# Optimization experiments

Measured on AMD Instinct MI355X. Metric: run time of the kernel, lower is better.

Reference implementation:

```python
import jax, jax.numpy as jnp
import numpy as np

B, D, H, W = 16, 512, 32, 32   # batch, input_dim, spatial
CD, K = 256, 8192              # codebook dim, num codes
COMMIT = 1.0


def setup_inputs() -> dict:
    key = jax.random.key(0)
    k0, k1, k2, k3 = jax.random.split(key, 4)
    x = jax.random.normal(k0, (B, D, H, W), dtype=jnp.float32)
    # project_in: Linear(D -> CD); project_out: Linear(CD -> D)
    W_in = jax.random.normal(k1, (CD, D), dtype=jnp.float32) * (1.0 / np.sqrt(D))
    b_in = jnp.zeros((CD,), dtype=jnp.float32)
    W_out = jax.random.normal(k2, (D, CD), dtype=jnp.float32) * (1.0 / np.sqrt(CD))
    b_out = jnp.zeros((D,), dtype=jnp.float32)
    codebook = jax.random.normal(k3, (K, CD), dtype=jnp.float32) * 0.05
    return {"x": x, "W_in": W_in, "b_in": b_in, "W_out": W_out,
            "b_out": b_out, "codebook": codebook}


def reference(x, W_in, b_in, W_out, b_out, codebook):
    b, d, h, w = x.shape
    # b d h w -> b (h w) d
    xt = x.reshape(b, d, h * w).transpose(0, 2, 1)
    z = xt @ W_in.T + b_in                              # [b, n, CD]
    # squared euclidean distances to all codes: ||z||^2 - 2 z.e + ||e||^2
    d2 = ((z * z).sum(-1, keepdims=True)
          - 2.0 * jnp.einsum('bnc,kc->bnk', z, codebook)
          + (codebook * codebook).sum(-1))              # [b, n, K]
    indices = jnp.argmin(d2, axis=-1)                   # [b, n] int
    q = codebook[indices]                               # [b, n, CD]
    # training branch: commitment loss + straight-through estimator
    commitment_loss = COMMIT * jnp.mean((jax.lax.stop_gradient(q) - z) ** 2)
    q_ste = z + jax.lax.stop_gradient(q - z)
    out = q_ste @ W_out.T + b_out                       # [b, n, d]
    out = out.transpose(0, 2, 1).reshape(b, d, h, w)    # b (h w) d -> b d h w
    return out, indices, commitment_loss
```

## Files before the change

kernel.cpp:

```cpp
#include <hip/hip_runtime.h>
#include <cfloat>
#include <cstdint>

#define B_      16
#define DIN     512
#define HW      1024
#define CDIM    256
#define KCODES  8192
#define NTOK    (B_ * HW)
#define OUT_ELEMS (B_ * DIN * HW)
#define NSTRIP  8
#define NPART2  16
#define CPS     (KCODES / NSTRIP)
#define MAXR    4096
#define RCHUNK  32
#define RBLOCKS 2048
#define LOSS_SCALE (1.0f / ((float)NTOK * (float)CDIM))
#define WSCALE      16.0f
#define INV_WS      0.0625f
#define INV_WS2     0.00390625f
#define NEG2_INV_WS (-0.125f)
#define BAND_SLACK  2e-3f
#define A_BYTES  131072
#define B_OFF    131072
#define EE_OFF   (131072 + 3 * 8192)
#define LDS_TOT  (EE_OFF + 4096)
#define PO_BOFF  65536
#define PO_TOT   163840

typedef __attribute__((ext_vector_type(8))) _Float16 f16x8;
typedef __attribute__((ext_vector_type(4))) float f32x4;

static __device__ __forceinline__ short f2h(float f) {
  _Float16 h = (_Float16)f;
  return __builtin_bit_cast(short, h);
}
static __device__ __forceinline__ float h2f(short h) {
  return (float)__builtin_bit_cast(_Float16, h);
}

#define GLL16(gsrc, ldst)                                                      \
  __builtin_amdgcn_global_load_lds(                                           \
      (const __attribute__((address_space(1))) unsigned int*)(gsrc),          \
      (__attribute__((address_space(3))) unsigned int*)(ldst), 16, 0, 0)

#define PREP_CB_BLKS 2048
#define PREP_W_BLKS  128
#define PREP_X_BLKS  2048
__global__ __launch_bounds__(256) void k_prep(
    const float* __restrict__ cb, const float* __restrict__ Win,
    const float* __restrict__ Wout, const float* __restrict__ x,
    short* __restrict__ cb_hi, short* __restrict__ cb_lo, float* __restrict__ ee,
    short* __restrict__ wi_hi, short* __restrict__ wi_lo,
    short* __restrict__ wo_hi,
    short* __restrict__ xT_hi, short* __restrict__ xT_lo,
    float* __restrict__ loss, int* __restrict__ rcount, int* __restrict__ scal) {
  __shared__ float T[64][65];
  const int blk = blockIdx.x;
  const int tid = threadIdx.x;
  if (blk == 0 && tid < 2) {
    if (tid == 0) *loss = 0.0f; else *rcount = 0;
  }
  if (blk < PREP_CB_BLKS) {
    const int wid = (blk * 256 + tid) >> 6;
    const int lane = tid & 63;
    const float4 v = *(const float4*)(cb + (size_t)wid * CDIM + lane * 4);
    float s = v.x * v.x + v.y * v.y + v.z * v.z + v.w * v.w;
    const float sx = v.x * WSCALE, sy = v.y * WSCALE,
                sz = v.z * WSCALE, sw = v.w * WSCALE;
    short4 h, l;
    h.x = f2h(sx); l.x = f2h(sx - h2f(h.x));
    h.y = f2h(sy); l.y = f2h(sy - h2f(h.y));
    h.z = f2h(sz); l.z = f2h(sz - h2f(h.z));
    h.w = f2h(sw); l.w = f2h(sw - h2f(h.w));
    *(short4*)(cb_hi + (size_t)wid * CDIM + lane * 4) = h;
    *(short4*)(cb_lo + (size_t)wid * CDIM + lane * 4) = l;
    const float rx = v.x - h2f(h.x) * INV_WS;
    const float ry = v.y - h2f(h.y) * INV_WS;
    const float rz = v.z - h2f(h.z) * INV_WS;
    const float rw = v.w - h2f(h.w) * INV_WS;
    float rr = rx * rx + ry * ry + rz * rz + rw * rw;
#pragma unroll
    for (int off = 32; off > 0; off >>= 1) {
      s += __shfl_down(s, off, 64);
      rr += __shfl_down(rr, off, 64);
    }
    const int wv = tid >> 6;
    if (lane == 0) { ee[wid] = s; T[0][wv] = s; T[1][wv] = rr; }
    __syncthreads();
    if (tid == 0) {
      const float em = fmaxf(fmaxf(T[0][0], T[0][1]), fmaxf(T[0][2], T[0][3]));
      const float rm = fmaxf(fmaxf(T[1][0], T[1][1]), fmaxf(T[1][2], T[1][3]));
      atomicMax(scal + 0, __float_as_int(em));
      atomicMax(scal + 1, __float_as_int(rm));
    }
  } else if (blk < PREP_CB_BLKS + PREP_W_BLKS) {
    const int i = ((blk - PREP_CB_BLKS) * 256 + tid) * 4;
    {
      const float4 v = *(const float4*)(Win + i);
      const float sx = v.x * WSCALE, sy = v.y * WSCALE,
                  sz = v.z * WSCALE, sw = v.w * WSCALE;
      short4 h, l;
      h.x = f2h(sx); l.x = f2h(sx - h2f(h.x));
      h.y = f2h(sy); l.y = f2h(sy - h2f(h.y));
      h.z = f2h(sz); l.z = f2h(sz - h2f(h.z));
      h.w = f2h(sw); l.w = f2h(sw - h2f(h.w));
      *(short4*)(wi_hi + i) = h; *(short4*)(wi_lo + i) = l;
    }
    {
      const float4 v = *(const float4*)(Wout + i);
      short4 h;
      h.x = f2h(v.x * WSCALE);
      h.y = f2h(v.y * WSCALE);
      h.z = f2h(v.z * WSCALE);
      h.w = f2h(v.w * WSCALE);
      *(short4*)(wo_hi + i) = h;
    }
  } else {
    const int id = blk - PREP_CB_BLKS - PREP_W_BLKS;
    const int xb = id & 255, yb = id >> 8;
    const int b = xb >> 4;
    const int hw0 = (xb & 15) * 64;
    const int din0 = yb * 64;
    {
      const int r = tid >> 2;
      const int c = tid & 3;
      const float* src = x + ((size_t)b * DIN + din0 + r) * HW + hw0 + c * 16;
#pragma unroll
      for (int j = 0; j < 4; ++j) {
        const float4 v = *(const float4*)(src + j * 4);
        T[r][c * 16 + j * 4 + 0] = v.x;
        T[r][c * 16 + j * 4 + 1] = v.y;
        T[r][c * 16 + j * 4 + 2] = v.z;
        T[r][c * 16 + j * 4 + 3] = v.w;
      }
    }
    __syncthreads();
    {
      const int tt = tid & 63;
      const int c2 = tid >> 6;
      short h[16], l[16];
#pragma unroll
      for (int j = 0; j < 16; ++j) {
        const float f = T[c2 * 16 + j][tt];
        h[j] = f2h(f); l[j] = f2h(f - h2f(h[j]));
      }
      const size_t base = ((size_t)b * HW + hw0 + tt) * DIN + din0 + c2 * 16;
      *(f16x8*)(xT_hi + base)     = *(f16x8*)&h[0];
      *(f16x8*)(xT_hi + base + 8) = *(f16x8*)&h[8];
      *(f16x8*)(xT_lo + base)     = *(f16x8*)&l[0];
      *(f16x8*)(xT_lo + base + 8) = *(f16x8*)&l[8];
    }
  }
}

__global__ __launch_bounds__(256, 2) void k_proj_in_mfma(
    const short* __restrict__ xT_hi, const short* __restrict__ xT_lo,
    const short* __restrict__ wi_hi, const short* __restrict__ wi_lo,
    const float* __restrict__ bin,
    short* __restrict__ z_hi, short* __restrict__ z_lo) {
  __shared__ short lds_s[3 * 16384];
  char* ldsc = (char*)lds_s;
  const int tid = threadIdx.x;
  const int w = tid >> 6, lane = tid & 63;
  const int quad = lane >> 4, l16 = lane & 15;
  const int wm = w >> 1, wn = w & 1;
  const int tok0 = blockIdx.x * 128;
  const int cd0 = blockIdx.y * 128;

  const int t0 = tid >> 2, p0 = tid & 3, q0 = p0 ^ ((t0 >> 1) & 3);
  const int u1 = tid + 256, t1 = u1 >> 2, p1 = u1 & 3, q1 = p1 ^ ((t1 >> 1) & 3);
  const short* A0h = xT_hi + (size_t)(tok0 + t0) * DIN + q0 * 8;
  const short* A1h = xT_hi + (size_t)(tok0 + t1) * DIN + q1 * 8;
  const short* A0l = xT_lo + (size_t)(tok0 + t0) * DIN + q0 * 8;
  const short* A1l = xT_lo + (size_t)(tok0 + t1) * DIN + q1 * 8;
  const short* B0h = wi_hi + (size_t)(cd0 + t0) * DIN + q0 * 8;
  const short* B1h = wi_hi + (size_t)(cd0 + t1) * DIN + q1 * 8;
  const short* B0l = wi_lo + (size_t)(cd0 + t0) * DIN + q0 * 8;
  const short* B1l = wi_lo + (size_t)(cd0 + t1) * DIN + q1 * 8;

#define PI_STAGE(s_, slot_)                                                    \
  {                                                                            \
    char* bb_ = ldsc + ((slot_) << 15);                                        \
    const int kb_ = (s_) * 32;                                                 \
    GLL16(A0h + kb_, bb_ + (w << 10));                                         \
    GLL16(A1h + kb_, bb_ + 4096 + (w << 10));                                  \
    GLL16(A0l + kb_, bb_ + 8192 + (w << 10));                                  \
    GLL16(A1l + kb_, bb_ + 12288 + (w << 10));                                 \
    GLL16(B0h + kb_, bb_ + 16384 + (w << 10));                                 \
    GLL16(B1h + kb_, bb_ + 20480 + (w << 10));                                 \
    GLL16(B0l + kb_, bb_ + 24576 + (w << 10));                                 \
    GLL16(B1l + kb_, bb_ + 28672 + (w << 10));                                 \
  }
  PI_STAGE(0, 0);
  PI_STAGE(1, 1);

  int aoffs[4], boffs[4];
#pragma unroll
  for (int mi = 0; mi < 4; ++mi) {
    const int t = wm * 64 + mi * 16 + l16;
    aoffs[mi] = t * 64 + (quad ^ ((t >> 1) & 3)) * 16;
  }
#pragma unroll
  for (int ni = 0; ni < 4; ++ni) {
    const int t = wn * 64 + ni * 16 + l16;
    boffs[ni] = 16384 + t * 64 + (quad ^ ((t >> 1) & 3)) * 16;
  }

  f32x4 acc[4][4];
#pragma unroll
  for (int mi = 0; mi < 4; ++mi)
#pragma unroll
    for (int ni = 0; ni < 4; ++ni) acc[mi][ni] = (f32x4){0.f, 0.f, 0.f, 0.f};

  int cur = 0;
#pragma unroll
  for (int s = 0; s < 16; ++s) {
    asm volatile("s_waitcnt vmcnt(8)" ::: "memory");
    __builtin_amdgcn_s_barrier();
    __builtin_amdgcn_sched_barrier(0);
    {
      const int s2 = (s + 2) & 15;
      const int nslot = cur + 2 - ((cur >= 1) ? 3 : 0);
      PI_STAGE(s2, nslot);
    }
    const int bb = cur << 15;
    f16x8 ah[4], al[4], bh[4], bl[4];
#pragma unroll
    for (int mi = 0; mi < 4; ++mi) {
      ah[mi] = *(const f16x8*)(ldsc + bb + aoffs[mi]);
      al[mi] = *(const f16x8*)(ldsc + bb + 8192 + aoffs[mi]);
    }
#pragma unroll
    for (int ni = 0; ni < 4; ++ni) {
      bh[ni] = *(const f16x8*)(ldsc + bb + boffs[ni]);
      bl[ni] = *(const f16x8*)(ldsc + bb + 8192 + boffs[ni]);
    }
    __builtin_amdgcn_s_setprio(1);
#pragma unroll
    for (int mi = 0; mi < 4; ++mi)
#pragma unroll
      for (int ni = 0; ni < 4; ++ni) {
        f32x4 c = acc[mi][ni];
        c = __builtin_amdgcn_mfma_f32_16x16x32_f16(ah[mi], bh[ni], c, 0, 0, 0);
        c = __builtin_amdgcn_mfma_f32_16x16x32_f16(ah[mi], bl[ni], c, 0, 0, 0);
        c = __builtin_amdgcn_mfma_f32_16x16x32_f16(al[mi], bh[ni], c, 0, 0, 0);
        acc[mi][ni] = c;
      }
    __builtin_amdgcn_s_setprio(0);
    cur = (cur == 2) ? 0 : cur + 1;
  }
#undef PI_STAGE

  float bv[4];
#pragma unroll
  for (int ni = 0; ni < 4; ++ni) bv[ni] = bin[cd0 + wn * 64 + ni * 16 + l16];
#pragma unroll
  for (int mi = 0; mi < 4; ++mi)
#pragma unroll
    for (int r = 0; r < 4; ++r) {
      const int t = tok0 + wm * 64 + mi * 16 + quad * 4 + r;
#pragma unroll
      for (int ni = 0; ni < 4; ++ni) {
        const int cd = cd0 + wn * 64 + ni * 16 + l16;
        const float o = acc[mi][ni][r] * INV_WS + bv[ni];
        const short h = f2h(o);
        z_hi[(size_t)t * CDIM + cd] = h;
        z_lo[(size_t)t * CDIM + cd] = f2h(o - h2f(h));
      }
    }
}

__global__ __launch_bounds__(512, 2) void k_argmin_mfma(
    const short* __restrict__ z_hi,
    const short* __restrict__ cb_hi,
    const float* __restrict__ ee,
    float* __restrict__ pm1v, int* __restrict__ pm1i, float* __restrict__ pm2v) {
  __shared__ short lds_s[LDS_TOT / 2];
  char* ldsc = (char*)lds_s;
  const int tid = threadIdx.x;
  const int w = tid >> 6, lane = tid & 63;
  const int quad = lane >> 4, l16 = lane & 15;
  const int wm = w >> 1, wn = w & 1;
  const int tok0 = blockIdx.x * 256;
  const int cbase = blockIdx.y * CPS;

#pragma unroll
  for (int r = 0; r < 16; ++r) {
    const int u = r * 512 + tid;
    const int c = u >> 10, t = (u >> 2) & 255, p = u & 3;
    const int q = p ^ ((t >> 1) & 3);
    GLL16(z_hi + (size_t)(tok0 + t) * CDIM + c * 32 + q * 8,
          ldsc + r * 8192 + (w << 10));
  }
  if (w < 4) {
    GLL16(ee + cbase + w * 256 + lane * 4, ldsc + EE_OFF + (w << 10));
  }
  const int crB = tid >> 2, pB = tid & 3;
  const int qB = pB ^ ((crB >> 1) & 3);
  const short* bsrc = cb_hi + (size_t)(cbase + crB) * CDIM + qB * 8;
  GLL16(bsrc, ldsc + B_OFF + (w << 10));
  GLL16(bsrc + 32, ldsc + B_OFF + 8192 + (w << 10));

  int aoffs[4], boffs[4];
#pragma unroll
  for (int mi = 0; mi < 4; ++mi) {
    const int t = wm * 64 + mi * 16 + l16;
    aoffs[mi] = t * 64 + (quad ^ ((t >> 1) & 3)) * 16;
  }
#pragma unroll
  for (int ni = 0; ni < 4; ++ni) {
    const int t = wn * 64 + ni * 16 + l16;
    boffs[ni] = t * 64 + (quad ^ ((t >> 1) & 3)) * 16;
  }
  const float* eelds = (const float*)(ldsc + EE_OFF);

  float mv[16], sv[16]; int mi_[16];
#pragma unroll
  for (int j = 0; j < 16; ++j) {
    mv[j] = FLT_MAX; sv[j] = FLT_MAX; mi_[j] = 0x7fffffff;
  }

  int cur = 0;
  for (int ct = 0; ct < 8; ++ct) {
    f32x4 acc[4][4];
#pragma unroll
    for (int mi = 0; mi < 4; ++mi)
#pragma unroll
      for (int ni = 0; ni < 4; ++ni) acc[mi][ni] = (f32x4){0.f, 0.f, 0.f, 0.f};

#pragma unroll
    for (int kbi = 0; kbi < 8; ++kbi) {
      const int s = ct * 8 + kbi;
      asm volatile("s_waitcnt vmcnt(1)" ::: "memory");
      __builtin_amdgcn_s_barrier();
      __builtin_amdgcn_sched_barrier(0);
      {
        const int s2 = (s + 2) & 63;
        const int nslot = cur + 2 - ((cur >= 1) ? 3 : 0);
        GLL16(bsrc + (size_t)(s2 >> 3) * 128 * CDIM + (s2 & 7) * 32,
              ldsc + B_OFF + (nslot << 13) + (w << 10));
      }
      const int abase = kbi << 14;
      const int bbase = B_OFF + (cur << 13);
      f16x8 ah[4], bh[4];
#pragma unroll
      for (int mi = 0; mi < 4; ++mi)
        ah[mi] = *(const f16x8*)(ldsc + abase + aoffs[mi]);
#pragma unroll
      for (int ni = 0; ni < 4; ++ni)
        bh[ni] = *(const f16x8*)(ldsc + bbase + boffs[ni]);
      __builtin_amdgcn_s_setprio(1);
#pragma unroll
      for (int mi = 0; mi < 4; ++mi)
#pragma unroll
        for (int ni = 0; ni < 4; ++ni)
          acc[mi][ni] = __builtin_amdgcn_mfma_f32_16x16x32_f16(
              ah[mi], bh[ni], acc[mi][ni], 0, 0, 0);
      __builtin_amdgcn_s_setprio(0);
      cur = (cur == 2) ? 0 : cur + 1;
    }
    const int ctile = cbase + ct * 128;
    float eev[4];
#pragma unroll
    for (int ni = 0; ni < 4; ++ni)
      eev[ni] = eelds[ct * 128 + wn * 64 + ni * 16 + l16];
    const int cb2 = ctile + wn * 64 + l16;
#pragma unroll
    for (int mi = 0; mi < 4; ++mi)
#pragma unroll
      for (int r = 0; r < 4; ++r) {
        const int j = mi * 4 + r;
#pragma unroll
        for (int ni = 0; ni < 4; ++ni) {
          const float s = fmaf(NEG2_INV_WS, acc[mi][ni][r], eev[ni]);
          sv[j] = fminf(sv[j], fmaxf(mv[j], s));
          if (s < mv[j]) { mv[j] = s; mi_[j] = cb2 + ni * 16; }
        }
      }
  }
#pragma unroll
  for (int off = 1; off < 16; off <<= 1) {
#pragma unroll
    for (int j = 0; j < 16; ++j) {
      const float ov = __shfl_xor(mv[j], off, 64);
      const int   oi = __shfl_xor(mi_[j], off, 64);
      const float os = __shfl_xor(sv[j], off, 64);
      const float snew = fminf(fminf(sv[j], os), fmaxf(mv[j], ov));
      if (ov < mv[j] || (ov == mv[j] && oi < mi_[j])) { mv[j] = ov; mi_[j] = oi; }
      sv[j] = snew;
    }
  }
  if (l16 == 0) {
    const int p = blockIdx.y * 2 + wn;
#pragma unroll
    for (int j = 0; j < 16; ++j) {
      const int mi = j >> 2, r = j & 3;
      const int t = tok0 + wm * 64 + mi * 16 + quad * 4 + r;
      const size_t o = (size_t)p * NTOK + t;
      pm1v[o] = mv[j]; pm1i[o] = mi_[j]; pm2v[o] = sv[j];
    }
  }
}

__global__ __launch_bounds__(256) void k_merge_rescue(
    const float* __restrict__ pm1v, const int* __restrict__ pm1i,
    const float* __restrict__ pm2v,
    const short* __restrict__ z_hi, const short* __restrict__ z_lo,
    const float* __restrict__ cb, const int* __restrict__ scal,
    int* __restrict__ idxi, float* __restrict__ idx_f,
    int* __restrict__ rlist, int* __restrict__ rcount,
    float* __restrict__ loss) {
  __shared__ float lpart[4];
  const int tid = threadIdx.x;
  const int wv = tid >> 6, lane = tid & 63;
  const int t = blockIdx.x * 4 + wv;
  float av = FLT_MAX, asv = FLT_MAX; int ai = 0x7fffffff;
  if (lane < NPART2) {
    const size_t po = (size_t)lane * NTOK + t;
    av = pm1v[po]; ai = pm1i[po]; asv = pm2v[po];
  }
  float m1v = av; int m1i = ai; float msv = asv;
#pragma unroll
  for (int off = 1; off < 64; off <<= 1) {
    const float ov = __shfl_xor(m1v, off, 64);
    const int   oi = __shfl_xor(m1i, off, 64);
    const float os = __shfl_xor(msv, off, 64);
    msv = fminf(msv, os);
    if (ov < m1v || (ov == m1v && oi < m1i)) { m1v = ov; m1i = oi; }
  }
  const short4 h4 = *(const short4*)(z_hi + (size_t)t * CDIM + lane * 4);
  const short4 l4 = *(const short4*)(z_lo + (size_t)t * CDIM + lane * 4);
  const float hx = h2f(h4.x), hy = h2f(h4.y), hz = h2f(h4.z), hw = h2f(h4.w);
  const float lx = h2f(l4.x), ly = h2f(l4.y), lz = h2f(l4.z), lw = h2f(l4.w);
  const float zx = hx + lx, zy = hy + ly, zz = hz + lz, zw = hw + lw;
  float zl2 = lx * lx + ly * ly + lz * lz + lw * lw;
  float zh2 = hx * hx + hy * hy + hz * hz + hw * hw;
#pragma unroll
  for (int off = 32; off > 0; off >>= 1) {
    zl2 += __shfl_xor(zl2, off, 64);
    zh2 += __shfl_xor(zh2, off, 64);
  }
  const float emax = sqrtf(__int_as_float(scal[0]));
  const float rmax = sqrtf(__int_as_float(scal[1]));
  const float band = 4.0f * (sqrtf(zl2) * emax + sqrtf(zh2) * rmax) + BAND_SLACK;
  const float thr = m1v + band;
  const unsigned long long ball = __ballot(av <= thr);
  const bool flag = (msv <= thr);
  int besti = m1i;
  if (__popcll(ball) > 1) {
    double bestv = 1e300; int bi = 0x7fffffff;
    unsigned long long bb = ball;
    while (bb) {
      const int c = __ffsll((long long)bb) - 1;
      bb &= bb - 1;
      const int ci = __shfl(ai, c, 64);
      const float4 ev = *(const float4*)(cb + (size_t)ci * CDIM + lane * 4);
      const double dx = (double)zx - (double)ev.x;
      const double dy = (double)zy - (double)ev.y;
      const double dz_ = (double)zz - (double)ev.z;
      const double dw = (double)zw - (double)ev.w;
      double d = dx * dx + dy * dy + dz_ * dz_ + dw * dw;
#pragma unroll
      for (int off = 32; off > 0; off >>= 1) d += __shfl_xor(d, off, 64);
      if (d < bestv || (d == bestv && ci < bi)) { bestv = d; bi = ci; }
    }
    besti = bi;
  }
  const float4 qv = *(const float4*)(cb + (size_t)besti * CDIM + lane * 4);
  const float dx = qv.x - zx;
  const float dy = qv.y - zy;
  const float dz_ = qv.z - zz;
  const float dw = qv.w - zw;
  float s = dx * dx + dy * dy + dz_ * dz_ + dw * dw;
#pragma unroll
  for (int off = 32; off > 0; off >>= 1) s += __shfl_down(s, off, 64);
  if (lane == 0) {
    idxi[t] = besti;
    idx_f[t] = (float)besti;
    lpart[wv] = s;
    if (flag) {
      const int pos = atomicAdd(rcount, 1);
      if (pos < MAXR) rlist[pos] = t;
    }
  }
  __syncthreads();
  if (tid == 0) {
    atomicAdd(loss, (lpart[0] + lpart[1] + lpart[2] + lpart[3]) * LOSS_SCALE);
  }
}

__global__ __launch_bounds__(256) void k_rescue_chunk(
    const short* __restrict__ z_hi, const short* __restrict__ z_lo,
    const float* __restrict__ cb,
    const int* __restrict__ rlist, const int* __restrict__ rcount,
    double* __restrict__ slotv, int* __restrict__ sloti) {
  const int cnt0 = *rcount;
  const int cnt = cnt0 < MAXR ? cnt0 : MAXR;
  const int li0 = blockIdx.x >> 5;
  const int chunk = blockIdx.x & (RCHUNK - 1);
  if (li0 >= cnt) return;
  __shared__ float zrow[CDIM];
  __shared__ double rv[256];
  __shared__ int ri[256];
  const int tid = threadIdx.x;
  for (int li = li0; li < cnt; li += RBLOCKS / RCHUNK) {
    const int t = rlist[li];
    zrow[tid] = h2f(z_hi[(size_t)t * CDIM + tid]) + h2f(z_lo[(size_t)t * CDIM + tid]);
    __syncthreads();
    const int k = chunk * 256 + tid;
    const float* e = cb + (size_t)k * CDIM;
    double s0 = 0.0, s1 = 0.0, s2 = 0.0, s3 = 0.0;
    for (int c = 0; c < CDIM; c += 4) {
      const float4 ev = *(const float4*)(e + c);
      const double d0 = (double)zrow[c]     - (double)ev.x;
      const double d1 = (double)zrow[c + 1] - (double)ev.y;
      const double d2 = (double)zrow[c + 2] - (double)ev.z;
      const double d3 = (double)zrow[c + 3] - (double)ev.w;
      s0 += d0 * d0; s1 += d1 * d1; s2 += d2 * d2; s3 += d3 * d3;
    }
    rv[tid] = (s0 + s1) + (s2 + s3);
    ri[tid] = k;
    __syncthreads();
    for (int off = 128; off > 0; off >>= 1) {
      if (tid < off) {
        if (rv[tid + off] < rv[tid] ||
            (rv[tid + off] == rv[tid] && ri[tid + off] < ri[tid])) {
          rv[tid] = rv[tid + off]; ri[tid] = ri[tid + off];
        }
      }
      __syncthreads();
    }
    if (tid == 0) {
      slotv[(size_t)li * RCHUNK + chunk] = rv[0];
      sloti[(size_t)li * RCHUNK + chunk] = ri[0];
    }
    __syncthreads();
  }
}

__global__ __launch_bounds__(256) void k_rescue_fin(
    const double* __restrict__ slotv, const int* __restrict__ sloti,
    const int* __restrict__ rlist, const int* __restrict__ rcount,
    const short* __restrict__ z_hi, const short* __restrict__ z_lo,
    const float* __restrict__ cb,
    int* __restrict__ idxi, float* __restrict__ idx_f, float* __restrict__ loss) {
  const int cnt0 = *rcount;
  const int cnt = cnt0 < MAXR ? cnt0 : MAXR;
  const int tid = threadIdx.x;
  const int wv = tid >> 6, lane = tid & 63;
  for (int li = wv; li < cnt; li += 4) {
    double bv = 1e300; int bx = 0x7fffffff;
    if (lane < RCHUNK) {
      bv = slotv[(size_t)li * RCHUNK + lane];
      bx = sloti[(size_t)li * RCHUNK + lane];
    }
#pragma unroll
    for (int off = 1; off < 32; off <<= 1) {
      const double ov = __shfl_xor(bv, off, 64);
      const int   oi = __shfl_xor(bx, off, 64);
      if (ov < bv || (ov == bv && oi < bx)) { bv = ov; bx = oi; }
    }
    const int newi = __shfl(bx, 0, 64);
    const int t = rlist[li];
    const int oldi = idxi[t];
    if (newi != oldi) {
      const short4 h4 = *(const short4*)(z_hi + (size_t)t * CDIM + lane * 4);
      const short4 l4 = *(const short4*)(z_lo + (size_t)t * CDIM + lane * 4);
      const float4 qn = *(const float4*)(cb + (size_t)newi * CDIM + lane * 4);
      const float4 qo = *(const float4*)(cb + (size_t)oldi * CDIM + lane * 4);
      const float zx = h2f(h4.x) + h2f(l4.x);
      const float zy = h2f(h4.y) + h2f(l4.y);
      const float zz = h2f(h4.z) + h2f(l4.z);
      const float zw = h2f(h4.w) + h2f(l4.w);
      float d = (qn.x - zx) * (qn.x - zx) - (qo.x - zx) * (qo.x - zx)
              + (qn.y - zy) * (qn.y - zy) - (qo.y - zy) * (qo.y - zy)
              + (qn.z - zz) * (qn.z - zz) - (qo.z - zz) * (qo.z - zz)
              + (qn.w - zw) * (qn.w - zw) - (qo.w - zw) * (qo.w - zw);
#pragma unroll
      for (int off = 32; off > 0; off >>= 1) d += __shfl_down(d, off, 64);
      if (lane == 0) {
        idxi[t] = newi;
        idx_f[t] = (float)newi;
        atomicAdd(loss, d * LOSS_SCALE);
      }
    }
  }
}

__global__ __launch_bounds__(512, 2) void k_proj_out_mfma(
    const short* __restrict__ wo_hi,
    const short* __restrict__ cb_hi, const short* __restrict__ cb_lo,
    const int* __restrict__ idxi, const float* __restrict__ bout,
    float* __restrict__ out) {
  __shared__ short lds_s[PO_TOT / 2];
  char* ldsc = (char*)lds_s;
  const int tid = threadIdx.x;
  const int w = tid >> 6, lane = tid & 63;
  const int quad = lane >> 4, l16 = lane & 15;
  const int wm = w >> 2, wn = w & 3;
  const int tok0 = blockIdx.x * 256;
  const int din0 = blockIdx.y * 128;

  const int tr = tid >> 2, p = tid & 3;
  const int q = p ^ ((tr >> 1) & 3);
  const int i0 = idxi[tok0 + tr];
  const int i1 = idxi[tok0 + 128 + tr];
  const short* s0h = cb_hi + (size_t)i0 * CDIM + q * 8;
  const short* s1h = cb_hi + (size_t)i1 * CDIM + q * 8;
  const short* s0l = cb_lo + (size_t)i0 * CDIM + q * 8;
  const short* s1l = cb_lo + (size_t)i1 * CDIM + q * 8;

#pragma unroll
  for (int c = 0; c < 8; ++c)
    GLL16(wo_hi + (size_t)(din0 + tr) * CDIM + c * 32 + q * 8,
          ldsc + c * 8192 + (w << 10));

#define PO_STAGE(s_, slot_)                                                    \
  {                                                                            \
    char* bb_ = ldsc + PO_BOFF + ((slot_) << 15);                              \
    GLL16(s0h + (s_) * 32, bb_ + (w << 10));                                   \
    GLL16(s1h + (s_) * 32, bb_ + 8192 + (w << 10));                            \
    GLL16(s0l + (s_) * 32, bb_ + 16384 + (w << 10));                           \
    GLL16(s1l + (s_) * 32, bb_ + 24576 + (w << 10));                           \
  }
  PO_STAGE(0, 0);
  PO_STAGE(1, 1);

  int aoffs[4], boffs[4];
#pragma unroll
  for (int mi = 0; mi < 4; ++mi) {
    const int t = wm * 64 + mi * 16 + l16;
    aoffs[mi] = t * 64 + (quad ^ ((t >> 1) & 3)) * 16;
  }
#pragma unroll
  for (int ni = 0; ni < 4; ++ni) {
    const int t = wn * 64 + ni * 16 + l16;
    boffs[ni] = t * 64 + (quad ^ ((t >> 1) & 3)) * 16;
  }

  f32x4 acc[4][4];
#pragma unroll
  for (int mi = 0; mi < 4; ++mi)
#pragma unroll
    for (int ni = 0; ni < 4; ++ni) acc[mi][ni] = (f32x4){0.f, 0.f, 0.f, 0.f};

  int cur = 0;
#pragma unroll
  for (int s = 0; s < 8; ++s) {
    asm volatile("s_waitcnt vmcnt(4)" ::: "memory");
    __builtin_amdgcn_s_barrier();
    __builtin_amdgcn_sched_barrier(0);
    {
      const int s2 = (s + 2) & 7;
      const int nslot = cur + 2 - ((cur >= 1) ? 3 : 0);
      PO_STAGE(s2, nslot);
    }
    const int abase = s << 13;
    const int bbase = PO_BOFF + (cur << 15);
    f16x8 ah[4], bh[4], bl[4];
#pragma unroll
    for (int mi = 0; mi < 4; ++mi)
      ah[mi] = *(const f16x8*)(ldsc + abase + aoffs[mi]);
#pragma unroll
    for (int ni = 0; ni < 4; ++ni) {
      bh[ni] = *(const f16x8*)(ldsc + bbase + boffs[ni]);
      bl[ni] = *(const f16x8*)(ldsc + bbase + 16384 + boffs[ni]);
    }
    __builtin_amdgcn_s_setprio(1);
#pragma unroll
    for (int mi = 0; mi < 4; ++mi)
#pragma unroll
      for (int ni = 0; ni < 4; ++ni) {
        f32x4 c = acc[mi][ni];
        c = __builtin_amdgcn_mfma_f32_16x16x32_f16(ah[mi], bh[ni], c, 0, 0, 0);
        c = __builtin_amdgcn_mfma_f32_16x16x32_f16(ah[mi], bl[ni], c, 0, 0, 0);
        acc[mi][ni] = c;
      }
    __builtin_amdgcn_s_setprio(0);
    cur = (cur == 2) ? 0 : cur + 1;
  }
#undef PO_STAGE

  const int b = tok0 >> 10;
  const int hwb = tok0 & (HW - 1);
  float* ob = out + (size_t)b * DIN * HW;
#pragma unroll
  for (int mi = 0; mi < 4; ++mi)
#pragma unroll
    for (int r = 0; r < 4; ++r) {
      const int din = din0 + wm * 64 + mi * 16 + quad * 4 + r;
      const float bb = bout[din];
#pragma unroll
      for (int ni = 0; ni < 4; ++ni) {
        const int hw = hwb + wn * 64 + ni * 16 + l16;
        ob[(size_t)din * HW + hw] = acc[mi][ni][r] * INV_WS2 + bb;
      }
    }
}

extern "C" void kernel_launch(void* const* d_in, const int* in_sizes, int n_in,
                              void* d_out, int out_size, void* d_ws, size_t ws_size,
                              hipStream_t stream) {
  const float* x    = (const float*)d_in[0];
  const float* Win  = (const float*)d_in[1];
  const float* bin  = (const float*)d_in[2];
  const float* Wout = (const float*)d_in[3];
  const float* bout = (const float*)d_in[4];
  const float* cb   = (const float*)d_in[5];

  float* out   = (float*)d_out;
  float* idx_f = out + OUT_ELEMS;
  float* loss  = out + OUT_ELEMS + NTOK;

  char* w = (char*)d_ws;
  size_t off = 0;
  short* z_hi  = (short*)(w + off); off += (size_t)NTOK * CDIM * 2;
  short* z_lo  = (short*)(w + off); off += (size_t)NTOK * CDIM * 2;
  short* cb_hi = (short*)(w + off); off += (size_t)KCODES * CDIM * 2;
  short* cb_lo = (short*)(w + off); off += (size_t)KCODES * CDIM * 2;
  short* xT_hi = (short*)(w + off); off += (size_t)NTOK * DIN * 2;
  short* xT_lo = (short*)(w + off); off += (size_t)NTOK * DIN * 2;
  short* wi_hi = (short*)(w + off); off += (size_t)CDIM * DIN * 2;
  short* wi_lo = (short*)(w + off); off += (size_t)CDIM * DIN * 2;
  short* wo_hi = (short*)(w + off); off += (size_t)DIN * CDIM * 2;
  float* ee    = (float*)(w + off); off += (size_t)KCODES * 4;
  int*   idxi  = (int*)(w + off);   off += (size_t)NTOK * 4;
  float* pm1v  = (float*)(w + off); off += (size_t)NPART2 * NTOK * 4;
  int*   pm1i  = (int*)(w + off);   off += (size_t)NPART2 * NTOK * 4;
  float* pm2v  = (float*)(w + off); off += (size_t)NPART2 * NTOK * 4;
  int*   rlist = (int*)(w + off);   off += (size_t)MAXR * 4;
  int*   rcount= (int*)(w + off);   off += 256;
  int*   scal  = (int*)(w + off);   off += 256;
  double* slotv= (double*)(w + off);off += (size_t)MAXR * RCHUNK * 8;
  int*   sloti = (int*)(w + off);   off += (size_t)MAXR * RCHUNK * 4;

  hipMemsetAsync(scal, 0, 8, stream);
  k_prep        <<<dim3(PREP_CB_BLKS + PREP_W_BLKS + PREP_X_BLKS),
                   dim3(256), 0, stream>>>(cb, Win, Wout, x, cb_hi, cb_lo, ee,
                                           wi_hi, wi_lo, wo_hi,
                                           xT_hi, xT_lo, loss, rcount, scal);
  k_proj_in_mfma<<<dim3(NTOK / 128, CDIM / 128), dim3(256), 0, stream>>>(
      xT_hi, xT_lo, wi_hi, wi_lo, bin, z_hi, z_lo);
  k_argmin_mfma <<<dim3(NTOK / 256, NSTRIP), dim3(512), 0, stream>>>(
      z_hi, cb_hi, ee, pm1v, pm1i, pm2v);
  k_merge_rescue<<<dim3(NTOK / 4), dim3(256), 0, stream>>>(
      pm1v, pm1i, pm2v, z_hi, z_lo, cb, scal, idxi, idx_f,
      rlist, rcount, loss);
  k_rescue_chunk<<<dim3(RBLOCKS), dim3(256), 0, stream>>>(
      z_hi, z_lo, cb, rlist, rcount, slotv, sloti);
  k_rescue_fin  <<<dim3(1), dim3(256), 0, stream>>>(
      slotv, sloti, rlist, rcount, z_hi, z_lo, cb, idxi, idx_f, loss);
  k_proj_out_mfma<<<dim3(NTOK / 256, DIN / 128), dim3(512), 0, stream>>>(
      wo_hi, cb_hi, cb_lo, idxi, bout, out);
}
```

Before: 429.9 us.

## Fuse rescue chunk and finalize kernels via last-block-done counter; drop setprio

```diff
diff --git a/kernel.cpp b/kernel.cpp
--- a/kernel.cpp
+++ b/kernel.cpp
@@ -54,12 +54,15 @@
     short* __restrict__ wi_hi, short* __restrict__ wi_lo,
     short* __restrict__ wo_hi,
     short* __restrict__ xT_hi, short* __restrict__ xT_lo,
-    float* __restrict__ loss, int* __restrict__ rcount, int* __restrict__ scal) {
+    float* __restrict__ loss, int* __restrict__ rcount,
+    int* __restrict__ done, int* __restrict__ scal) {
   __shared__ float T[64][65];
   const int blk = blockIdx.x;
   const int tid = threadIdx.x;
-  if (blk == 0 && tid < 2) {
-    if (tid == 0) *loss = 0.0f; else *rcount = 0;
+  if (blk == 0 && tid < 3) {
+    if (tid == 0) *loss = 0.0f;
+    else if (tid == 1) *rcount = 0;
+    else *done = 0;
   }
   if (blk < PREP_CB_BLKS) {
     const int wid = (blk * 256 + tid) >> 6;
@@ -350,14 +353,12 @@
 #pragma unroll
       for (int ni = 0; ni < 4; ++ni)
         bh[ni] = *(const f16x8*)(ldsc + bbase + boffs[ni]);
-      __builtin_amdgcn_s_setprio(1);
 #pragma unroll
       for (int mi = 0; mi < 4; ++mi)
 #pragma unroll
         for (int ni = 0; ni < 4; ++ni)
           acc[mi][ni] = __builtin_amdgcn_mfma_f32_16x16x32_f16(
               ah[mi], bh[ni], acc[mi][ni], 0, 0, 0);
-      __builtin_amdgcn_s_setprio(0);
       cur = (cur == 2) ? 0 : cur + 1;
     }
     const int ctile = cbase + ct * 128;
@@ -490,64 +491,63 @@
   }
 }
 
-__global__ __launch_bounds__(256) void k_rescue_chunk(
+__global__ __launch_bounds__(256) void k_rescue_fused(
     const short* __restrict__ z_hi, const short* __restrict__ z_lo,
     const float* __restrict__ cb,
     const int* __restrict__ rlist, const int* __restrict__ rcount,
-    double* __restrict__ slotv, int* __restrict__ sloti) {
+    double* __restrict__ slotv, int* __restrict__ sloti,
+    int* __restrict__ done,
+    int* __restrict__ idxi, float* __restrict__ idx_f,
+    float* __restrict__ loss) {
   const int cnt0 = *rcount;
   const int cnt = cnt0 < MAXR ? cnt0 : MAXR;
   const int li0 = blockIdx.x >> 5;
   const int chunk = blockIdx.x & (RCHUNK - 1);
-  if (li0 >= cnt) return;
   __shared__ float zrow[CDIM];
   __shared__ double rv[256];
   __shared__ int ri[256];
+  __shared__ int lastFlag;
   const int tid = threadIdx.x;
-  for (int li = li0; li < cnt; li += RBLOCKS / RCHUNK) {
-    const int t = rlist[li];
-    zrow[tid] = h2f(z_hi[(size_t)t * CDIM + tid]) + h2f(z_lo[(size_t)t * CDIM + tid]);
-    __syncthreads();
-    const int k = chunk * 256 + tid;
-    const float* e = cb + (size_t)k * CDIM;
-    double s0 = 0.0, s1 = 0.0, s2 = 0.0, s3 = 0.0;
-    for (int c = 0; c < CDIM; c += 4) {
-      const float4 ev = *(const float4*)(e + c);
-      const double d0 = (double)zrow[c]     - (double)ev.x;
-      const double d1 = (double)zrow[c + 1] - (double)ev.y;
-      const double d2 = (double)zrow[c + 2] - (double)ev.z;
-      const double d3 = (double)zrow[c + 3] - (double)ev.w;
-      s0 += d0 * d0; s1 += d1 * d1; s2 += d2 * d2; s3 += d3 * d3;
-    }
-    rv[tid] = (s0 + s1) + (s2 + s3);
-    ri[tid] = k;
-    __syncthreads();
-    for (int off = 128; off > 0; off >>= 1) {
-      if (tid < off) {
-        if (rv[tid + off] < rv[tid] ||
-            (rv[tid + off] == rv[tid] && ri[tid + off] < ri[tid])) {
-          rv[tid] = rv[tid + off]; ri[tid] = ri[tid + off];
+  if (li0 < cnt) {
+    for (int li = li0; li < cnt; li += RBLOCKS / RCHUNK) {
+      const int t = rlist[li];
+      zrow[tid] = h2f(z_hi[(size_t)t * CDIM + tid]) + h2f(z_lo[(size_t)t * CDIM + tid]);
+      __syncthreads();
+      const int k = chunk * 256 + tid;
+      const float* e = cb + (size_t)k * CDIM;
+      double s0 = 0.0, s1 = 0.0, s2 = 0.0, s3 = 0.0;
+      for (int c = 0; c < CDIM; c += 4) {
+        const float4 ev = *(const float4*)(e + c);
+        const double d0 = (double)zrow[c]     - (double)ev.x;
+        const double d1 = (double)zrow[c + 1] - (double)ev.y;
+        const double d2 = (double)zrow[c + 2] - (double)ev.z;
+        const double d3 = (double)zrow[c + 3] - (double)ev.w;
+        s0 += d0 * d0; s1 += d1 * d1; s2 += d2 * d2; s3 += d3 * d3;
+      }
+      rv[tid] = (s0 + s1) + (s2 + s3);
+      ri[tid] = k;
+      __syncthreads();
+      for (int off = 128; off > 0; off >>= 1) {
+        if (tid < off) {
+          if (rv[tid + off] < rv[tid] ||
+              (rv[tid + off] == rv[tid] && ri[tid + off] < ri[tid])) {
+            rv[tid] = rv[tid + off]; ri[tid] = ri[tid + off];
+          }
         }
+        __syncthreads();
+      }
+      if (tid == 0) {
+        slotv[(size_t)li * RCHUNK + chunk] = rv[0];
+        sloti[(size_t)li * RCHUNK + chunk] = ri[0];
       }
       __syncthreads();
     }
-    if (tid == 0) {
-      slotv[(size_t)li * RCHUNK + chunk] = rv[0];
-      sloti[(size_t)li * RCHUNK + chunk] = ri[0];
-    }
-    __syncthreads();
-  }
-}
-
-__global__ __launch_bounds__(256) void k_rescue_fin(
-    const double* __restrict__ slotv, const int* __restrict__ sloti,
-    const int* __restrict__ rlist, const int* __restrict__ rcount,
-    const short* __restrict__ z_hi, const short* __restrict__ z_lo,
-    const float* __restrict__ cb,
-    int* __restrict__ idxi, float* __restrict__ idx_f, float* __restrict__ loss) {
-  const int cnt0 = *rcount;
-  const int cnt = cnt0 < MAXR ? cnt0 : MAXR;
-  const int tid = threadIdx.x;
+  }
+  __threadfence();
+  if (tid == 0) lastFlag = (atomicAdd(done, 1) == RBLOCKS - 1);
+  __syncthreads();
+  if (lastFlag == 0) return;
+  __threadfence();
   const int wv = tid >> 6, lane = tid & 63;
   for (int li = wv; li < cnt; li += 4) {
     double bv = 1e300; int bx = 0x7fffffff;
@@ -731,6 +731,7 @@
   float* pm2v  = (float*)(w + off); off += (size_t)NPART2 * NTOK * 4;
   int*   rlist = (int*)(w + off);   off += (size_t)MAXR * 4;
   int*   rcount= (int*)(w + off);   off += 256;
+  int*   done  = (int*)(w + off);   off += 256;
   int*   scal  = (int*)(w + off);   off += 256;
   double* slotv= (double*)(w + off);off += (size_t)MAXR * RCHUNK * 8;
   int*   sloti = (int*)(w + off);   off += (size_t)MAXR * RCHUNK * 4;
@@ -739,7 +740,8 @@
   k_prep        <<<dim3(PREP_CB_BLKS + PREP_W_BLKS + PREP_X_BLKS),
                    dim3(256), 0, stream>>>(cb, Win, Wout, x, cb_hi, cb_lo, ee,
                                            wi_hi, wi_lo, wo_hi,
-                                           xT_hi, xT_lo, loss, rcount, scal);
+                                           xT_hi, xT_lo, loss, rcount, done,
+                                           scal);
   k_proj_in_mfma<<<dim3(NTOK / 128, CDIM / 128), dim3(256), 0, stream>>>(
       xT_hi, xT_lo, wi_hi, wi_lo, bin, z_hi, z_lo);
   k_argmin_mfma <<<dim3(NTOK / 256, NSTRIP), dim3(512), 0, stream>>>(
@@ -747,10 +749,8 @@
   k_merge_rescue<<<dim3(NTOK / 4), dim3(256), 0, stream>>>(
       pm1v, pm1i, pm2v, z_hi, z_lo, cb, scal, idxi, idx_f,
       rlist, rcount, loss);
-  k_rescue_chunk<<<dim3(RBLOCKS), dim3(256), 0, stream>>>(
-      z_hi, z_lo, cb, rlist, rcount, slotv, sloti);
-  k_rescue_fin  <<<dim3(1), dim3(256), 0, stream>>>(
-      slotv, sloti, rlist, rcount, z_hi, z_lo, cb, idxi, idx_f, loss);
+  k_rescue_fused<<<dim3(RBLOCKS), dim3(256), 0, stream>>>(
+      z_hi, z_lo, cb, rlist, rcount, slotv, sloti, done, idxi, idx_f, loss);
   k_proj_out_mfma<<<dim3(NTOK / 256, DIN / 128), dim3(512), 0, stream>>>(
       wo_hi, cb_hi, cb_lo, idxi, bout, out);
 }
```

Result: slower. 536.8 us (+24.9%).
